# Kernel optimization log

Measured on AMD Instinct MI355X. Metric: run time of the kernel, lower is better.

## Reference

```python
import jax, jax.numpy as jnp
import numpy as np

DEPTH = 2
DIM = 256
MLP = 1024
B = 2
N = 2048


def setup_inputs() -> dict:
    key = jax.random.key(0)
    ks = jax.random.split(key, 6)
    s = 0.02
    d = DIM
    f32 = jnp.float32
    return {
        "x": jax.random.normal(ks[0], (B, N, d), f32),
        "ln1_g": jnp.ones((DEPTH, d), f32),
        "ln1_b": jnp.zeros((DEPTH, d), f32),
        "Wqkv": (jax.random.normal(ks[1], (DEPTH, d, 3 * d), f32) * s),
        "bqkv": jnp.zeros((DEPTH, 3 * d), f32),
        "Wo": (jax.random.normal(ks[2], (DEPTH, d, d), f32) * s),
        "bo": jnp.zeros((DEPTH, d), f32),
        "ln2_g": jnp.ones((DEPTH, d), f32),
        "ln2_b": jnp.zeros((DEPTH, d), f32),
        "W1": (jax.random.normal(ks[3], (DEPTH, d, MLP), f32) * s),
        "b1": jnp.zeros((DEPTH, MLP), f32),
        "W2": (jax.random.normal(ks[4], (DEPTH, MLP, d), f32) * s),
        "b2": jnp.zeros((DEPTH, d), f32),
        "heads": 8,
    }


def _ln(x, g, b, eps=1e-5):
    m = x.mean(-1, keepdims=True)
    v = ((x - m) ** 2).mean(-1, keepdims=True)
    return (x - m) * jax.lax.rsqrt(v + eps) * g + b


def reference(x, ln1_g, ln1_b, Wqkv, bqkv, Wo, bo, ln2_g, ln2_b, W1, b1, W2, b2, heads):
    b, n, dim = x.shape
    hd = dim // heads
    scale = hd ** -0.5
    depth = Wqkv.shape[0]
    out = x
    # NOTE: faithful to original: `x` is never updated inside the loop,
    # so only the last layer's output is returned.
    for i in range(depth):
        y = _ln(x, ln1_g[i], ln1_b[i])
        qkv = y @ Wqkv[i] + bqkv[i]                      # [b,n,3*dim]
        qkv = qkv.reshape(b, n, 3, heads, hd)
        q, k, v = jnp.moveaxis(qkv, 2, 0)                # each [b,n,h,hd]
        q = q.transpose(0, 2, 1, 3)                      # [b,h,n,hd]
        k = k.transpose(0, 2, 1, 3)
        v = v.transpose(0, 2, 1, 3)
        dots = jnp.einsum('bhid,bhjd->bhij', q, k) * scale
        attn = jax.nn.softmax(dots, axis=-1)
        o = jnp.einsum('bhij,bhjd->bhid', attn, v)       # [b,h,n,hd]
        o = o.transpose(0, 2, 1, 3).reshape(b, n, dim)
        o = o @ Wo[i] + bo[i]
        a = o + x                                        # attn residual
        z = _ln(a, ln2_g[i], ln2_b[i])
        m = jax.nn.gelu(z @ W1[i] + b1[i], approximate=False) @ W2[i] + b2[i]
        out = m + a                                      # mlp residual
    return out
```

## Files before the change

kernel.cpp:

```cpp
#include <hip/hip_runtime.h>
#include <hip/hip_bf16.h>
#include <math.h>

#define DEPTHC 2
#define DIMD   256
#define MLPD   1024
#define BB     2
#define NN     2048
#define HH     8
#define HD     32
#define ROWS   (BB * NN)

typedef __attribute__((ext_vector_type(8))) short bf16x8;
typedef __attribute__((ext_vector_type(4))) float f32x4;

__device__ __forceinline__ short f2bf(float x) {
    union { float f; unsigned u; } c; c.f = x;
    unsigned u = c.u + (0x7fffu + ((c.u >> 16) & 1u));
    return (short)(u >> 16);
}
__device__ __forceinline__ float bf2f(short s) {
    union { unsigned u; float f; } c; c.u = ((unsigned)(unsigned short)s) << 16;
    return c.f;
}

__global__ __launch_bounds__(256) void prep(
    const float* __restrict__ Wqkv, const float* __restrict__ Wo,
    const float* __restrict__ W1,   const float* __restrict__ W2,
    short* __restrict__ WqkvF, short* __restrict__ WoF,
    short* __restrict__ W1F,   short* __restrict__ W2F,
    const float* __restrict__ x, const float* __restrict__ g,
    const float* __restrict__ be, short* __restrict__ y)
{
    __shared__ short Ts[128][72];

    if (blockIdx.x >= 96) {
        const int wave = threadIdx.x >> 6;
        const int lane = threadIdx.x & 63;
        const int row  = (blockIdx.x - 96) * 4 + wave;
        const int c    = lane * 4;

        const float4 v = *(const float4*)&x[(size_t)row * DIMD + c];
        float s  = v.x + v.y + v.z + v.w;
        float sq = v.x * v.x + v.y * v.y + v.z * v.z + v.w * v.w;
#pragma unroll
        for (int off = 32; off > 0; off >>= 1) {
            s  += __shfl_down(s,  off, 64);
            sq += __shfl_down(sq, off, 64);
        }
        s  = __shfl(s,  0, 64);
        sq = __shfl(sq, 0, 64);

        const float mean = s * (1.f / DIMD);
        const float var  = sq * (1.f / DIMD) - mean * mean;
        const float rstd = rsqrtf(var + 1e-5f);

        const float4 gg = *(const float4*)&g[c];
        const float4 bb = *(const float4*)&be[c];
        short4 ov;
        ov.x = f2bf((v.x - mean) * rstd * gg.x + bb.x);
        ov.y = f2bf((v.y - mean) * rstd * gg.y + bb.y);
        ov.z = f2bf((v.z - mean) * rstd * gg.z + bb.z);
        ov.w = f2bf((v.w - mean) * rstd * gg.w + bb.w);
        *(short4*)&y[(size_t)row * DIMD + c] = ov;
        return;
    }

    int blk = blockIdx.x;
    const float* W; short* WF; int K, N;
    if (blk < 24)      {           W = Wqkv; WF = WqkvF; K = 256;  N = 768;  }
    else if (blk < 32) { blk -= 24; W = Wo;   WF = WoF;   K = 256;  N = 256;  }
    else if (blk < 64) { blk -= 32; W = W1;   WF = W1F;   K = 256;  N = 1024; }
    else               { blk -= 64; W = W2;   WF = W2F;   K = 1024; N = 256;  }
    const int nkc = K >> 7;
    const int bx  = blk / nkc;
    const int kc  = blk % nkc;
    const int n0  = bx * 64;
    const int k0  = kc * 128;

    const int nc  = threadIdx.x & 63;
    const int kr0 = threadIdx.x >> 6;
#pragma unroll
    for (int i = 0; i < 32; ++i) {
        const int kr = kr0 + i * 4;
        Ts[kr][nc] = f2bf(W[(size_t)(k0 + kr) * N + n0 + nc]);
    }
    __syncthreads();

    short* out = WF + ((size_t)bx * nkc + kc) * 8192;
#pragma unroll
    for (int i = 0; i < 4; ++i) {
        const int u    = threadIdx.x + i * 256;
        const int l16  = u & 15;
        const int quad = (u >> 4) & 3;
        const int nt   = (u >> 6) & 3;
        const int ks   = (u >> 8) & 3;
        const int n    = nt * 16 + l16;
        const int kk   = (ks * 4 + quad) * 8;
        bf16x8 v;
#pragma unroll
        for (int j = 0; j < 8; ++j) v[j] = Ts[kk + j][n];
        *(bf16x8*)&out[(size_t)u * 8] = v;
    }
}

template <int K, bool GELU, bool RES, bool OBF, bool VTG>
__global__ __launch_bounds__(256) void gemm_ks(
    const short* __restrict__ A, const short* __restrict__ WF,
    const float* __restrict__ bias, const float* __restrict__ R,
    void* __restrict__ Cv, int N, short* __restrict__ vtg)
{
    __shared__ short smem[4][4096];

    const int tid  = threadIdx.x;
    const int w    = tid >> 6;
    const int lane = tid & 63;
    const int quad = lane >> 4;
    const int l16  = lane & 15;
    const int n0   = blockIdx.x * 64;
    const int m0   = blockIdx.y * 64;
    constexpr int NKC   = K / 128;
    constexpr int SLICE = K / 4;
    constexpr int NHC   = SLICE / 64;

    const short* wfb  = WF + (size_t)blockIdx.x * NKC * 8192;
    const short* arow = A + (size_t)(m0 + l16) * K + quad * 8;
    short* reg = smem[w];

    f32x4 acc[4][4] = {};

#pragma unroll
    for (int hc = 0; hc < NHC; ++hc) {
        const int kbase = w * SLICE + hc * 64;
        const short* src = wfb +
            ((size_t)(kbase >> 7) * 1024 + (size_t)((kbase >> 6) & 1) * 512) * 8;
#pragma unroll
        for (int i = 0; i < 8; ++i)
            *(bf16x8*)&reg[(i * 64 + lane) * 8] =
                *(const bf16x8*)&src[(size_t)(i * 64 + lane) * 8];

#pragma unroll
        for (int ksl = 0; ksl < 2; ++ksl) {
            const int kk = kbase + ksl * 32;
            bf16x8 af[4];
#pragma unroll
            for (int mt = 0; mt < 4; ++mt)
                af[mt] = *(const bf16x8*)(arow + (size_t)mt * 16 * K + kk);
#pragma unroll
            for (int nt = 0; nt < 4; ++nt) {
                const bf16x8 bf = *(const bf16x8*)
                    &reg[(((ksl * 4 + nt) * 4 + quad) * 16 + l16) * 8];
#pragma unroll
                for (int mt = 0; mt < 4; ++mt)
                    acc[mt][nt] = __builtin_amdgcn_mfma_f32_16x16x32_bf16(
                        af[mt], bf, acc[mt][nt], 0, 0, 0);
            }
        }
    }

#pragma unroll
    for (int p = 0; p < 2; ++p) {
        __syncthreads();
#pragma unroll
        for (int mtl = 0; mtl < 2; ++mtl)
#pragma unroll
            for (int nt = 0; nt < 4; ++nt)
                *(f32x4*)&smem[w][((mtl * 4 + nt) * 64 + lane) * 8] = acc[2 * p + mtl][nt];
        __syncthreads();
        if ((w >> 1) == p) {
            const int mtl = w & 1;
            const int mt  = 2 * p + mtl;
#pragma unroll
            for (int nt = 0; nt < 4; ++nt) {
                const int idx = ((mtl * 4 + nt) * 64 + lane) * 8;
                const f32x4 s0 = *(const f32x4*)&smem[0][idx];
                const f32x4 s1 = *(const f32x4*)&smem[1][idx];
                const f32x4 s2 = *(const f32x4*)&smem[2][idx];
                const f32x4 s3 = *(const f32x4*)&smem[3][idx];
                const f32x4 s  = (s0 + s1) + (s2 + s3);
                const int col  = n0 + nt * 16 + l16;
                const float bb = bias[col];
#pragma unroll
                for (int r = 0; r < 4; ++r) {
                    const int row = m0 + mt * 16 + quad * 4 + r;
                    float v = s[r] + bb;
                    if (RES)  v += R[(size_t)row * N + col];
                    if (GELU) v = 0.5f * v * (1.f + erff(v * 0.70710678118f));
                    const short bv = f2bf(v);
                    if (OBF) ((short*)Cv)[(size_t)row * N + col] = bv;
                    else     ((float*)Cv)[(size_t)row * N + col] = v;
                    if (VTG && n0 >= 2 * DIMD) {
                        const int vc = col - 2 * DIMD;
                        const int b  = row >> 11;
                        const int q  = row & (NN - 1);
                        const int h  = vc >> 5;
                        const int d  = vc & 31;
                        vtg[((size_t)(b * HH + h) * HD + d) * NN + q] = bv;
                    }
                }
            }
        }
    }
}

__global__ __launch_bounds__(256) void ln_kernel(
    const float* __restrict__ x, const float* __restrict__ g,
    const float* __restrict__ bta, short* __restrict__ y)
{
    const int wave = threadIdx.x >> 6;
    const int lane = threadIdx.x & 63;
    const int row  = blockIdx.x * 4 + wave;
    const int c    = lane * 4;

    const float4 v = *(const float4*)&x[(size_t)row * DIMD + c];
    float s  = v.x + v.y + v.z + v.w;
    float sq = v.x * v.x + v.y * v.y + v.z * v.z + v.w * v.w;
#pragma unroll
    for (int off = 32; off > 0; off >>= 1) {
        s  += __shfl_down(s,  off, 64);
        sq += __shfl_down(sq, off, 64);
    }
    s  = __shfl(s,  0, 64);
    sq = __shfl(sq, 0, 64);

    const float mean = s * (1.f / DIMD);
    const float var  = sq * (1.f / DIMD) - mean * mean;
    const float rstd = rsqrtf(var + 1e-5f);

    const float4 gg = *(const float4*)&g[c];
    const float4 bb = *(const float4*)&bta[c];
    short4 ov;
    ov.x = f2bf((v.x - mean) * rstd * gg.x + bb.x);
    ov.y = f2bf((v.y - mean) * rstd * gg.y + bb.y);
    ov.z = f2bf((v.z - mean) * rstd * gg.z + bb.z);
    ov.w = f2bf((v.w - mean) * rstd * gg.w + bb.w);
    *(short4*)&y[(size_t)row * DIMD + c] = ov;
}

__global__ __launch_bounds__(256) void attn_mfma(
    const short* __restrict__ qkv, const short* __restrict__ vtg,
    short* __restrict__ o)
{
    __shared__ short Ks[64][40];
    __shared__ short Vs[32][72];
    __shared__ short Ps[4][16][72];

    const int tid  = threadIdx.x;
    const int w    = tid >> 6;
    const int lane = tid & 63;
    const int quad = lane >> 4;
    const int l16  = lane & 15;
    const int bh   = blockIdx.y;
    const int b    = bh >> 3;
    const int h    = bh & 7;
    const int q0   = blockIdx.x * 64 + w * 16;

    const float scale = 0.17677669529663689f;
    const float shift = 11.090354888959125f;
    const short* base = qkv + (size_t)b * NN * (3 * DIMD);

    const bf16x8 qfrag =
        *(const bf16x8*)(base + (size_t)(q0 + l16) * (3 * DIMD) + h * HD + quad * 8);

    const int skey = tid >> 2;
    const int sd   = (tid & 3) * 8;
    const int vd   = tid >> 3;
    const int vk   = (tid & 7) * 8;

    const short* kgp = base + (size_t)skey * (3 * DIMD) + DIMD + h * HD + sd;
    const short* vgp = vtg + ((size_t)bh * HD + vd) * NN + vk;

    f32x4 oacc0 = {0.f, 0.f, 0.f, 0.f};
    f32x4 oacc1 = {0.f, 0.f, 0.f, 0.f};
    float rowsum = 0.f;

    bf16x8 kreg = *(const bf16x8*)kgp;
    bf16x8 vreg = *(const bf16x8*)vgp;

#pragma unroll 1
    for (int t = 0; t < NN / 64; ++t) {
        __syncthreads();
        *(bf16x8*)&Ks[skey][sd] = kreg;
        *(bf16x8*)&Vs[vd][vk]   = vreg;
        __syncthreads();

        if (t + 1 < NN / 64) {
            kreg = *(const bf16x8*)(kgp + (size_t)(t + 1) * 64 * (3 * DIMD));
            vreg = *(const bf16x8*)(vgp + (t + 1) * 64);
        }

        f32x4 s[4];
#pragma unroll
        for (int kt = 0; kt < 4; ++kt) {
            const bf16x8 kf = *(const bf16x8*)&Ks[kt * 16 + l16][quad * 8];
            f32x4 z = {0.f, 0.f, 0.f, 0.f};
            s[kt] = __builtin_amdgcn_mfma_f32_16x16x32_bf16(kf, qfrag, z, 0, 0, 0);
        }

#pragma unroll
        for (int kt = 0; kt < 4; ++kt) {
            short4 pv;
#pragma unroll
            for (int r = 0; r < 4; ++r) {
                const float p = __expf(fmaf(s[kt][r], scale, -shift));
                rowsum += p;
                union { float f; unsigned u; } cv; cv.f = p;
                ((short*)&pv)[r] = (short)(cv.u >> 16);
            }
            *(short4*)&Ps[w][l16][kt * 16 + quad * 4] = pv;
        }

#pragma unroll
        for (int c = 0; c < 2; ++c) {
            const bf16x8 pf = *(const bf16x8*)&Ps[w][l16][c * 32 + quad * 8];
            const bf16x8 v0 = *(const bf16x8*)&Vs[l16][c * 32 + quad * 8];
            const bf16x8 v1 = *(const bf16x8*)&Vs[16 + l16][c * 32 + quad * 8];
            oacc0 = __builtin_amdgcn_mfma_f32_16x16x32_bf16(pf, v0, oacc0, 0, 0, 0);
            oacc1 = __builtin_amdgcn_mfma_f32_16x16x32_bf16(pf, v1, oacc1, 0, 0, 0);
        }
    }

    rowsum += __shfl_xor(rowsum, 16, 64);
    rowsum += __shfl_xor(rowsum, 32, 64);

#pragma unroll
    for (int r = 0; r < 4; ++r) {
        const float L   = __shfl(rowsum, quad * 4 + r, 16);
        const float inv = 1.f / L;
        const size_t row = (size_t)(b * NN + q0 + quad * 4 + r);
        o[row * DIMD + h * HD + l16]      = f2bf(oacc0[r] * inv);
        o[row * DIMD + h * HD + 16 + l16] = f2bf(oacc1[r] * inv);
    }
}

extern "C" void kernel_launch(void* const* d_in, const int* in_sizes, int n_in,
                              void* d_out, int out_size, void* d_ws, size_t ws_size,
                              hipStream_t stream)
{
    const int L = DEPTHC - 1;
    const float* x     = (const float*)d_in[0];
    const float* ln1_g = (const float*)d_in[1]  + L * DIMD;
    const float* ln1_b = (const float*)d_in[2]  + L * DIMD;
    const float* Wqkv  = (const float*)d_in[3]  + (size_t)L * DIMD * 3 * DIMD;
    const float* bqkv  = (const float*)d_in[4]  + L * 3 * DIMD;
    const float* Wo    = (const float*)d_in[5]  + (size_t)L * DIMD * DIMD;
    const float* bo    = (const float*)d_in[6]  + L * DIMD;
    const float* ln2_g = (const float*)d_in[7]  + L * DIMD;
    const float* ln2_b = (const float*)d_in[8]  + L * DIMD;
    const float* W1    = (const float*)d_in[9]  + (size_t)L * DIMD * MLPD;
    const float* b1    = (const float*)d_in[10] + L * MLPD;
    const float* W2    = (const float*)d_in[11] + (size_t)L * MLPD * DIMD;
    const float* b2    = (const float*)d_in[12] + L * DIMD;
    float* out = (float*)d_out;

    short* WqkvF = (short*)d_ws;
    short* WoF   = WqkvF + 12 * 2 * 8192;
    short* W1F   = WoF   + 4 * 2 * 8192;
    short* W2F   = W1F   + 16 * 2 * 8192;
    short* ybf   = W2F   + 4 * 8 * 8192;
    short* zbf   = ybf   + (size_t)ROWS * DIMD;
    short* qkvbf = zbf   + (size_t)ROWS * DIMD;
    short* vtg   = qkvbf + (size_t)ROWS * 3 * DIMD;
    short* obf   = vtg   + (size_t)16 * HD * NN;
    short* m1bf  = obf   + (size_t)ROWS * DIMD;
    float* a     = (float*)(m1bf + (size_t)ROWS * MLPD);

    prep<<<96 + ROWS / 4, 256, 0, stream>>>(
        Wqkv, Wo, W1, W2, WqkvF, WoF, W1F, W2F, x, ln1_g, ln1_b, ybf);

    gemm_ks<256, false, false, true, true><<<dim3(12, 64), 256, 0, stream>>>(
        ybf, WqkvF, bqkv, nullptr, qkvbf, 3 * DIMD, vtg);

    attn_mfma<<<dim3(NN / 64, BB * HH), 256, 0, stream>>>(qkvbf, vtg, obf);

    gemm_ks<256, false, true, false, false><<<dim3(4, 64), 256, 0, stream>>>(
        obf, WoF, bo, x, a, DIMD, nullptr);

    ln_kernel<<<ROWS / 4, 256, 0, stream>>>(a, ln2_g, ln2_b, zbf);

    gemm_ks<256, true, false, true, false><<<dim3(16, 64), 256, 0, stream>>>(
        zbf, W1F, b1, nullptr, m1bf, MLPD, nullptr);

    gemm_ks<1024, false, true, false, false><<<dim3(4, 64), 256, 0, stream>>>(
        m1bf, W2F, b2, a, out, DIMD, nullptr);
}
```

Baseline: 165.4 us.

## Split attention key range across wave pairs and merge partial results

Each attention block now handles 32 queries instead of 64. Its four waves form two query groups by two key halves, each processing half of the 2048 keys, and the partial outputs and row sums are combined through shared memory at the end. This doubles the grid to give more blocks and shorter per-block loops for better occupancy and latency hiding. The cost is an extra LDS reduction, two more barriers, and K/V tiles that are loaded once per 32 queries instead of once per 64. The merge is valid without rescaling because softmax uses a fixed exponent shift.

```diff
diff --git a/kernel.cpp b/kernel.cpp
--- a/kernel.cpp
+++ b/kernel.cpp
@@ -241,19 +241,21 @@
     const short* __restrict__ qkv, const short* __restrict__ vtg,
     short* __restrict__ o)
 {
-    __shared__ short Ks[64][40];
-    __shared__ short Vs[32][72];
-    __shared__ short Ps[4][16][72];
+    __shared__ __align__(16) short Ks2[2][64][40];
+    __shared__ __align__(16) short Vs2[2][32][72];
+    __shared__ __align__(16) short Ps[4][16][72];
 
     const int tid  = threadIdx.x;
     const int w    = tid >> 6;
     const int lane = tid & 63;
     const int quad = lane >> 4;
     const int l16  = lane & 15;
+    const int qw    = w & 1;
+    const int kside = w >> 1;
     const int bh   = blockIdx.y;
     const int b    = bh >> 3;
     const int h    = bh & 7;
-    const int q0   = blockIdx.x * 64 + w * 16;
+    const int q0   = blockIdx.x * 32 + qw * 16;
 
     const float scale = 0.17677669529663689f;
     const float shift = 11.090354888959125f;
@@ -262,37 +264,48 @@
     const bf16x8 qfrag =
         *(const bf16x8*)(base + (size_t)(q0 + l16) * (3 * DIMD) + h * HD + quad * 8);
 
-    const int skey = tid >> 2;
-    const int sd   = (tid & 3) * 8;
-    const int vd   = tid >> 3;
-    const int vk   = (tid & 7) * 8;
-
-    const short* kgp = base + (size_t)skey * (3 * DIMD) + DIMD + h * HD + sd;
-    const short* vgp = vtg + ((size_t)bh * HD + vd) * NN + vk;
+    const int side = tid >> 7;
+    const int st   = tid & 127;
+    const int kr   = st >> 1;
+    const int kd   = (st & 1) * 16;
+    const int vd   = st >> 2;
+    const int vk0  = (st & 3) * 16;
+
+    const short* kgp = base + (size_t)(side * 1024 + kr) * (3 * DIMD)
+                       + DIMD + h * HD + kd;
+    const short* vgp = vtg + ((size_t)bh * HD + vd) * NN + side * 1024 + vk0;
 
     f32x4 oacc0 = {0.f, 0.f, 0.f, 0.f};
     f32x4 oacc1 = {0.f, 0.f, 0.f, 0.f};
     float rowsum = 0.f;
 
-    bf16x8 kreg = *(const bf16x8*)kgp;
-    bf16x8 vreg = *(const bf16x8*)vgp;
+    bf16x8 kr0 = *(const bf16x8*)kgp;
+    bf16x8 kr1 = *(const bf16x8*)(kgp + 8);
+    bf16x8 vr0 = *(const bf16x8*)vgp;
+    bf16x8 vr1 = *(const bf16x8*)(vgp + 8);
 
 #pragma unroll 1
-    for (int t = 0; t < NN / 64; ++t) {
+    for (int t = 0; t < NN / 128; ++t) {
         __syncthreads();
-        *(bf16x8*)&Ks[skey][sd] = kreg;
-        *(bf16x8*)&Vs[vd][vk]   = vreg;
+        *(bf16x8*)&Ks2[side][kr][kd]     = kr0;
+        *(bf16x8*)&Ks2[side][kr][kd + 8] = kr1;
+        *(bf16x8*)&Vs2[side][vd][vk0]     = vr0;
+        *(bf16x8*)&Vs2[side][vd][vk0 + 8] = vr1;
         __syncthreads();
 
-        if (t + 1 < NN / 64) {
-            kreg = *(const bf16x8*)(kgp + (size_t)(t + 1) * 64 * (3 * DIMD));
-            vreg = *(const bf16x8*)(vgp + (t + 1) * 64);
+        if (t + 1 < NN / 128) {
+            const short* kn = kgp + (size_t)(t + 1) * 64 * (3 * DIMD);
+            const short* vn = vgp + (t + 1) * 64;
+            kr0 = *(const bf16x8*)kn;
+            kr1 = *(const bf16x8*)(kn + 8);
+            vr0 = *(const bf16x8*)vn;
+            vr1 = *(const bf16x8*)(vn + 8);
         }
 
         f32x4 s[4];
 #pragma unroll
         for (int kt = 0; kt < 4; ++kt) {
-            const bf16x8 kf = *(const bf16x8*)&Ks[kt * 16 + l16][quad * 8];
+            const bf16x8 kf = *(const bf16x8*)&Ks2[kside][kt * 16 + l16][quad * 8];
             f32x4 z = {0.f, 0.f, 0.f, 0.f};
             s[kt] = __builtin_amdgcn_mfma_f32_16x16x32_bf16(kf, qfrag, z, 0, 0, 0);
         }
@@ -313,8 +326,8 @@
 #pragma unroll
         for (int c = 0; c < 2; ++c) {
             const bf16x8 pf = *(const bf16x8*)&Ps[w][l16][c * 32 + quad * 8];
-            const bf16x8 v0 = *(const bf16x8*)&Vs[l16][c * 32 + quad * 8];
-            const bf16x8 v1 = *(const bf16x8*)&Vs[16 + l16][c * 32 + quad * 8];
+            const bf16x8 v0 = *(const bf16x8*)&Vs2[kside][l16][c * 32 + quad * 8];
+            const bf16x8 v1 = *(const bf16x8*)&Vs2[kside][16 + l16][c * 32 + quad * 8];
             oacc0 = __builtin_amdgcn_mfma_f32_16x16x32_bf16(pf, v0, oacc0, 0, 0, 0);
             oacc1 = __builtin_amdgcn_mfma_f32_16x16x32_bf16(pf, v1, oacc1, 0, 0, 0);
         }
@@ -323,13 +336,29 @@
     rowsum += __shfl_xor(rowsum, 16, 64);
     rowsum += __shfl_xor(rowsum, 32, 64);
 
-#pragma unroll
-    for (int r = 0; r < 4; ++r) {
-        const float L   = __shfl(rowsum, quad * 4 + r, 16);
-        const float inv = 1.f / L;
-        const size_t row = (size_t)(b * NN + q0 + quad * 4 + r);
-        o[row * DIMD + h * HD + l16]      = f2bf(oacc0[r] * inv);
-        o[row * DIMD + h * HD + 16 + l16] = f2bf(oacc1[r] * inv);
+    float* sc = (float*)&Ks2[0][0][0];
+    __syncthreads();
+    if (kside == 1) {
+        float* o8 = sc + (size_t)(qw * 64 + lane) * 8;
+        *(f32x4*)o8       = oacc0;
+        *(f32x4*)(o8 + 4) = oacc1;
+        if (lane < 16) sc[1024 + qw * 16 + lane] = rowsum;
+    }
+    __syncthreads();
+    if (kside == 0) {
+        const float* o8 = sc + (size_t)(qw * 64 + lane) * 8;
+        oacc0 += *(const f32x4*)o8;
+        oacc1 += *(const f32x4*)(o8 + 4);
+        rowsum += sc[1024 + qw * 16 + l16];
+
+#pragma unroll
+        for (int r = 0; r < 4; ++r) {
+            const float L   = __shfl(rowsum, quad * 4 + r, 16);
+            const float inv = 1.f / L;
+            const size_t row = (size_t)(b * NN + q0 + quad * 4 + r);
+            o[row * DIMD + h * HD + l16]      = f2bf(oacc0[r] * inv);
+            o[row * DIMD + h * HD + 16 + l16] = f2bf(oacc1[r] * inv);
+        }
     }
 }
 
@@ -371,7 +400,7 @@
     gemm_ks<256, false, false, true, true><<<dim3(12, 64), 256, 0, stream>>>(
         ybf, WqkvF, bqkv, nullptr, qkvbf, 3 * DIMD, vtg);
 
-    attn_mfma<<<dim3(NN / 64, BB * HH), 256, 0, stream>>>(qkvbf, vtg, obf);
+    attn_mfma<<<dim3(NN / 32, BB * HH), 256, 0, stream>>>(qkvbf, vtg, obf);
 
     gemm_ks<256, false, true, false, false><<<dim3(4, 64), 256, 0, stream>>>(
         obf, WoF, bo, x, a, DIMD, nullptr);
```

New measurement: 162.5 us. About the same (-1.7%).
